# Kernel optimization log

Measured on AMD Instinct MI355X. Metric: run time of the kernel, lower is better.

The kernel has to match this reference:

```python
import jax, jax.numpy as jnp
import numpy as np

N = 8192      # number of tree nodes
IN = 1024     # in_dim
M = 1024      # effective mem_dim = 2 * mem_dim_init
K = 8         # max children (complete 8-ary tree)


def _linear_init(key, out_dim, in_dim):
    k1, k2 = jax.random.split(key)
    s = 1.0 / np.sqrt(in_dim)
    w = jax.random.uniform(k1, (out_dim, in_dim), minval=-s, maxval=s, dtype=jnp.float32)
    b = jax.random.uniform(k2, (out_dim,), minval=-s, maxval=s, dtype=jnp.float32)
    return w, b


def setup_inputs() -> dict:
    key = jax.random.key(0)
    ks = jax.random.split(key, 5)
    w_ioux, b_ioux = _linear_init(ks[0], 3 * M, IN)
    w_iouh, b_iouh = _linear_init(ks[1], 3 * M, M)
    w_fx, b_fx = _linear_init(ks[2], M, IN)
    w_fh, b_fh = _linear_init(ks[3], M, M)
    inputs = jax.random.normal(ks[4], (N, IN), dtype=jnp.float32)
    # Complete K-ary tree: children of node p are p*K+1 .. p*K+K (clipped).
    # Pad with index N, which addresses an always-zero dummy row.
    ch = np.full((N, K), N, dtype=np.int32)
    for j in range(K):
        idx = np.arange(N) * K + 1 + j
        valid = idx < N
        ch[valid, j] = idx[valid]
    return dict(inputs=inputs, children=jnp.asarray(ch),
                w_ioux=w_ioux, b_ioux=b_ioux, w_iouh=w_iouh, b_iouh=b_iouh,
                w_fx=w_fx, b_fx=b_fx, w_fh=w_fh, b_fh=b_fh)


def reference(inputs, children, w_ioux, b_ioux, w_iouh, b_iouh, w_fx, b_fx, w_fh, b_fh):
    # Precompute the input-side projections for all nodes at once.
    iou_x = inputs @ w_ioux.T + b_ioux   # [N, 3M]
    fx_x = inputs @ w_fx.T + b_fx        # [N, M]
    h0 = jnp.zeros((N + 1, M), inputs.dtype)  # row N is the zero pad slot
    c0 = jnp.zeros((N + 1, M), inputs.dtype)

    def step(carry, t):
        h_buf, c_buf = carry
        ch = children[t]           # [K] child indices (pad = N -> zero rows)
        ch_h = h_buf[ch]           # [K, M] real child h's
        ch_c = c_buf[ch]           # [K, M] real child c's
        # Faithful to original: for internal nodes child_c/child_h are SWAPPED,
        # so the 'child_h_sum' and f-gate inputs use the real c's, while the
        # forgotten memory (fc) multiplies the real h's. Leaves: all zeros.
        csum = ch_c.sum(0)                                   # [M]
        iou = iou_x[t] + csum @ w_iouh.T + b_iouh            # [3M]
        i_g, o_g, u_g = jnp.split(iou, 3)
        i_g = jax.nn.sigmoid(i_g)
        o_g = jax.nn.sigmoid(o_g)
        u_g = jnp.tanh(u_g)
        f = jax.nn.sigmoid(ch_c @ w_fh.T + b_fh + fx_x[t])   # [K, M]
        c = i_g * u_g + (f * ch_h).sum(0)                    # [M]
        h = o_g * jnp.tanh(c)
        return (h_buf.at[t].set(h), c_buf.at[t].set(c)), None

    # Children always have larger indices than their parent, so processing
    # t = N-1 .. 0 matches the original reverse-BFS (leaves-first) order.
    order = jnp.arange(N - 1, -1, -1)
    (h_buf, c_buf), _ = jax.lax.scan(step, (h0, c0), order)
    root_h = h_buf[0][None, :]   # [1, M]
    root_c = c_buf[0][None, :]   # [1, M]
    return root_h, root_c
```

## Files before the change

kernel.cpp:

```cpp
#include <hip/hip_runtime.h>

typedef __bf16 bf16x8 __attribute__((ext_vector_type(8)));
typedef __attribute__((ext_vector_type(4))) float f4;

#define AS1 __attribute__((address_space(1)))
#define AS3 __attribute__((address_space(3)))

__device__ __forceinline__ unsigned short f2bf(float f) {
    union { float f; unsigned int u; } x; x.f = f;
    return (unsigned short)((x.u + 0x7fffu + ((x.u >> 16) & 1u)) >> 16);
}
__device__ __forceinline__ float bf2f(unsigned short u) {
    union { unsigned int u; float f; } x; x.u = (unsigned int)u << 16;
    return x.f;
}
__device__ __forceinline__ float fsigm(float x) {
    return __builtin_amdgcn_rcpf(1.f + __expf(-x));
}
__device__ __forceinline__ float ftanh(float x) {
    return 1.f - 2.f * __builtin_amdgcn_rcpf(1.f + __expf(2.f * x));
}
__device__ __forceinline__ void gload_lds16(const unsigned short* g, unsigned short* l) {
    __builtin_amdgcn_global_load_lds((const AS1 unsigned int*)g, (AS3 unsigned int*)l, 16, 0, 0);
}

__global__ void prep_all_k(const float* __restrict__ inputs, const float* __restrict__ w_ioux,
                           const float* __restrict__ w_fx, const float* __restrict__ w_iouh,
                           const float* __restrict__ w_fh,
                           const float* __restrict__ b_ioux, const float* __restrict__ b_iouh,
                           const float* __restrict__ b_fx, const float* __restrict__ b_fh,
                           unsigned short* __restrict__ Xbf, unsigned short* __restrict__ Wiouxbf,
                           unsigned short* __restrict__ Wfxbf, unsigned short* __restrict__ Whbf,
                           unsigned short* __restrict__ Wfhbf,
                           float* __restrict__ bias_iou, float* __restrict__ bias_f,
                           unsigned short* __restrict__ c_bf, unsigned short* __restrict__ h_bf) {
    int b = blockIdx.x;
    if (b < 16384) {
        int idx = b * 256 + threadIdx.x;
        const float* src; unsigned short* dst; int rel;
        if (idx < 2097152)      { src = inputs; dst = Xbf;     rel = idx; }
        else if (idx < 2883584) { src = w_ioux; dst = Wiouxbf; rel = idx - 2097152; }
        else if (idx < 3145728) { src = w_fx;   dst = Wfxbf;   rel = idx - 2883584; }
        else if (idx < 3932160) { src = w_iouh; dst = Whbf;    rel = idx - 3145728; }
        else                    { src = w_fh;   dst = Wfhbf;   rel = idx - 3932160; }
        float4 v = reinterpret_cast<const float4*>(src)[rel];
        ushort4 o; o.x = f2bf(v.x); o.y = f2bf(v.y); o.z = f2bf(v.z); o.w = f2bf(v.w);
        reinterpret_cast<ushort4*>(dst)[rel] = o;
    } else if (b < 16400) {
        int idx = (b - 16384) * 256 + threadIdx.x;
        if (idx < 3072) bias_iou[idx] = b_ioux[idx] + b_iouh[idx];
        else { int j = idx - 3072; bias_f[j] = b_fx[j] + b_fh[j]; }
    } else {
        int j = (b - 16400) * 256 + threadIdx.x;
        size_t o = (size_t)8192 * 1024 + j;
        c_bf[o] = 0; h_bf[o] = 0;
    }
}

__device__ __forceinline__ void gemm_core_db(const unsigned short* __restrict__ A,
                                             const unsigned short* __restrict__ B,
                                             int M, int tile_m, int tile_n, int kb, int nsteps,
                                             unsigned short* lsA, unsigned short* lsB,
                                             f4 acc[4][4]) {
    const int K = 1024;
    const int tid = threadIdx.x;
    const int l = tid & 63, wid = tid >> 6;
    const int wm = wid >> 1, wn = wid & 1;
    const int fr = l & 15, q = l >> 4;

#pragma unroll
    for (int i = 0; i < 4; ++i)
#pragma unroll
        for (int j = 0; j < 4; ++j) acc[i][j] = (f4){0.f, 0.f, 0.f, 0.f};

    const unsigned short* ga[4]; const unsigned short* gb[4];
    unsigned short *la[4], *lb[4];
#pragma unroll
    for (int i = 0; i < 4; ++i) {
        int chunk = i * 256 + tid;
        int row = chunk >> 3, slot = chunk & 7;
        int scol = (slot ^ (row & 7)) * 8;
        ga[i] = A + (size_t)min(tile_m + row, M - 1) * K + kb * 64 + scol;
        gb[i] = B + (size_t)(tile_n + row) * K + kb * 64 + scol;
        la[i] = lsA + chunk * 8;
        lb[i] = lsB + chunk * 8;
    }
#pragma unroll
    for (int i = 0; i < 4; ++i) gload_lds16(ga[i], la[i]);
#pragma unroll
    for (int i = 0; i < 4; ++i) gload_lds16(gb[i], lb[i]);

    int roffA[4], roffB[4];
#pragma unroll
    for (int f = 0; f < 4; ++f) {
        roffA[f] = (wm * 64 + f * 16 + fr) * 64;
        roffB[f] = (wn * 64 + f * 16 + fr) * 64;
    }
    const int sw = fr & 7;
    int cur = 0;
    for (int t = 0; t < nsteps; ++t) {
        if (t < nsteps - 1) {
            int k0 = (t + 1) * 64;
            int nb = (cur ^ 1) * 8192;
#pragma unroll
            for (int i = 0; i < 4; ++i) gload_lds16(ga[i] + k0, la[i] + nb);
#pragma unroll
            for (int i = 0; i < 4; ++i) gload_lds16(gb[i] + k0, lb[i] + nb);
            asm volatile("s_waitcnt vmcnt(8)" ::: "memory");
        } else {
            asm volatile("s_waitcnt vmcnt(0)" ::: "memory");
        }
        __builtin_amdgcn_s_barrier();
        const unsigned short* bA = lsA + cur * 8192;
        const unsigned short* bB = lsB + cur * 8192;
        bf16x8 af[4][2], bq[4][2];
#pragma unroll
        for (int f = 0; f < 4; ++f)
#pragma unroll
            for (int s = 0; s < 2; ++s) {
                int sl = ((s * 4 + q) ^ sw) * 8;
                af[f][s] = *reinterpret_cast<const bf16x8*>(&bA[roffA[f] + sl]);
                bq[f][s] = *reinterpret_cast<const bf16x8*>(&bB[roffB[f] + sl]);
            }
#pragma unroll
        for (int s = 0; s < 2; ++s)
#pragma unroll
            for (int i = 0; i < 4; ++i)
#pragma unroll
                for (int j = 0; j < 4; ++j)
                    acc[i][j] = __builtin_amdgcn_mfma_f32_16x16x32_bf16(af[i][s], bq[j][s], acc[i][j], 0, 0, 0);
        __builtin_amdgcn_s_barrier();
        cur ^= 1;
    }
}

__global__ __launch_bounds__(256)
void gemm_big_k(const unsigned short* __restrict__ Xbf, const unsigned short* __restrict__ Wioux,
                const unsigned short* __restrict__ Wfx,
                const float* __restrict__ bias_iou, const float* __restrict__ bias_f,
                unsigned short* __restrict__ P_iou, unsigned short* __restrict__ P_f) {
    __shared__ unsigned short lsA[16384];
    __shared__ unsigned short lsB[16384];
    int b = blockIdx.x;
    const unsigned short* Bp; unsigned short* Cp; const float* biasp;
    int ldc, tm, tn, M;
    if (b < 1536) {
        tm = (b & 63) * 128; tn = (b >> 6) * 128;
        Bp = Wioux; Cp = P_iou; biasp = bias_iou; ldc = 3072; M = 8192;
    } else {
        int bb = b - 1536;
        tm = (bb & 7) * 128; tn = (bb >> 3) * 128;
        Bp = Wfx; Cp = P_f; biasp = bias_f; ldc = 1024; M = 1024;
    }
    f4 acc[4][4];
    gemm_core_db(Xbf, Bp, M, tm, tn, 0, 16, lsA, lsB, acc);

    const int l = threadIdx.x & 63, wid = threadIdx.x >> 6;
    const int wm = wid >> 1, wn = wid & 1;
    const int fr = l & 15, q = l >> 4;
#pragma unroll
    for (int i = 0; i < 4; ++i)
#pragma unroll
        for (int j = 0; j < 4; ++j) {
            int col = tn + wn * 64 + fr + j * 16;
            float bv = biasp[col];
#pragma unroll
            for (int r = 0; r < 4; ++r) {
                int row = tm + wm * 64 + q * 4 + i * 16 + r;
                Cp[(size_t)row * ldc + col] = f2bf(acc[i][j][r] + bv);
            }
        }
}

__global__ void leaf_act_k(const unsigned short* __restrict__ P_iou,
                           unsigned short* __restrict__ h_bf, unsigned short* __restrict__ c_bf) {
    int idx = blockIdx.x * blockDim.x + threadIdx.x;
    int t = 1024 + (idx >> 8);
    int j = (idx & 255) * 4;
    const unsigned short* p = P_iou + (size_t)t * 3072 + j;
    ushort4 pi = *reinterpret_cast<const ushort4*>(p);
    ushort4 po = *reinterpret_cast<const ushort4*>(p + 1024);
    ushort4 pu = *reinterpret_cast<const ushort4*>(p + 2048);
    ushort4 cb, hb;
    float c0, c1, c2, c3;
    c0 = fsigm(bf2f(pi.x)) * ftanh(bf2f(pu.x)); hb.x = f2bf(fsigm(bf2f(po.x)) * ftanh(c0)); cb.x = f2bf(c0);
    c1 = fsigm(bf2f(pi.y)) * ftanh(bf2f(pu.y)); hb.y = f2bf(fsigm(bf2f(po.y)) * ftanh(c1)); cb.y = f2bf(c1);
    c2 = fsigm(bf2f(pi.z)) * ftanh(bf2f(pu.z)); hb.z = f2bf(fsigm(bf2f(po.z)) * ftanh(c2)); cb.z = f2bf(c2);
    c3 = fsigm(bf2f(pi.w)) * ftanh(bf2f(pu.w)); hb.w = f2bf(fsigm(bf2f(po.w)) * ftanh(c3)); cb.w = f2bf(c3);
    size_t o = (size_t)t * 1024 + j;
    *reinterpret_cast<ushort4*>(c_bf + o) = cb;
    *reinterpret_cast<ushort4*>(h_bf + o) = hb;
}

__device__ __forceinline__ void csum_dev(const unsigned short* __restrict__ c_bf,
                                         unsigned short* __restrict__ csum_bf, int lo, int w) {
    int tt = w >> 8, j = (w & 255) * 4;
    int t = lo + tt;
    size_t base = (size_t)(t * 8 + 1) * 1024 + j;
    float s0 = 0.f, s1 = 0.f, s2 = 0.f, s3 = 0.f;
#pragma unroll
    for (int k = 0; k < 8; ++k) {
        ushort4 v = *reinterpret_cast<const ushort4*>(c_bf + base + (size_t)k * 1024);
        s0 += bf2f(v.x); s1 += bf2f(v.y); s2 += bf2f(v.z); s3 += bf2f(v.w);
    }
    ushort4 o; o.x = f2bf(s0); o.y = f2bf(s1); o.z = f2bf(s2); o.w = f2bf(s3);
    *reinterpret_cast<ushort4*>(csum_bf + (size_t)t * 1024 + j) = o;
}

__global__ void csum_k(const unsigned short* __restrict__ c_bf, unsigned short* __restrict__ csum_bf,
                       int lo, int n) {
    int w = blockIdx.x * blockDim.x + threadIdx.x;
    if (w < n * 256) csum_dev(c_bf, csum_bf, lo, w);
}

__global__ void node_update_k(const unsigned short* __restrict__ P_iou,
                              const unsigned short* __restrict__ P_f,
                              const float* __restrict__ out_iouh, const float* __restrict__ out_f,
                              unsigned short* __restrict__ h_bf, unsigned short* __restrict__ c_bf,
                              float* __restrict__ out, int lo, int n) {
    int w = blockIdx.x * blockDim.x + threadIdx.x;
    if (w >= n * 256) return;
    int tt = w >> 8, j = (w & 255) * 4;
    int t = lo + tt;
    const unsigned short* p = P_iou + (size_t)t * 3072 + j;
    ushort4 pi4 = *reinterpret_cast<const ushort4*>(p);
    ushort4 po4 = *reinterpret_cast<const ushort4*>(p + 1024);
    ushort4 pu4 = *reinterpret_cast<const ushort4*>(p + 2048);
    const float* oi = out_iouh + (size_t)tt * 3072 + j;
    f4 oii = *reinterpret_cast<const f4*>(oi);
    f4 oio = *reinterpret_cast<const f4*>(oi + 1024);
    f4 oiu = *reinterpret_cast<const f4*>(oi + 2048);
    ushort4 pf4 = *reinterpret_cast<const ushort4*>(P_f + (size_t)t * 1024 + j);
    float pf[4] = {bf2f(pf4.x), bf2f(pf4.y), bf2f(pf4.z), bf2f(pf4.w)};
    float a[4], og[4];
    a[0] = fsigm(bf2f(pi4.x) + oii[0]) * ftanh(bf2f(pu4.x) + oiu[0]);
    a[1] = fsigm(bf2f(pi4.y) + oii[1]) * ftanh(bf2f(pu4.y) + oiu[1]);
    a[2] = fsigm(bf2f(pi4.z) + oii[2]) * ftanh(bf2f(pu4.z) + oiu[2]);
    a[3] = fsigm(bf2f(pi4.w) + oii[3]) * ftanh(bf2f(pu4.w) + oiu[3]);
    og[0] = fsigm(bf2f(po4.x) + oio[0]);
    og[1] = fsigm(bf2f(po4.y) + oio[1]);
    og[2] = fsigm(bf2f(po4.z) + oio[2]);
    og[3] = fsigm(bf2f(po4.w) + oio[3]);
#pragma unroll
    for (int k = 0; k < 8; ++k) {
        f4 fo = *reinterpret_cast<const f4*>(out_f + (size_t)(tt * 8 + k) * 1024 + j);
        ushort4 hc = *reinterpret_cast<const ushort4*>(h_bf + (size_t)(t * 8 + 1 + k) * 1024 + j);
        a[0] += fsigm(pf[0] + fo[0]) * bf2f(hc.x);
        a[1] += fsigm(pf[1] + fo[1]) * bf2f(hc.y);
        a[2] += fsigm(pf[2] + fo[2]) * bf2f(hc.z);
        a[3] += fsigm(pf[3] + fo[3]) * bf2f(hc.w);
    }
    float h0 = og[0] * ftanh(a[0]);
    float h1 = og[1] * ftanh(a[1]);
    float h2 = og[2] * ftanh(a[2]);
    float h3 = og[3] * ftanh(a[3]);
    size_t o = (size_t)t * 1024 + j;
    ushort4 cb; cb.x = f2bf(a[0]); cb.y = f2bf(a[1]); cb.z = f2bf(a[2]); cb.w = f2bf(a[3]);
    ushort4 hb; hb.x = f2bf(h0); hb.y = f2bf(h1); hb.z = f2bf(h2); hb.w = f2bf(h3);
    *reinterpret_cast<ushort4*>(c_bf + o) = cb;
    *reinterpret_cast<ushort4*>(h_bf + o) = hb;
    if (t == 0) {
        f4 hv = {h0, h1, h2, h3};
        f4 cv = {a[0], a[1], a[2], a[3]};
        *reinterpret_cast<f4*>(out + j) = hv;
        *reinterpret_cast<f4*>(out + 1024 + j) = cv;
    }
}

struct GDesc {
    const unsigned short* A;
    const unsigned short* B;
    float* C;
    int M;
    int ldc;
    int tiles_n;
    int tiles_total;
};

__global__ __launch_bounds__(256)
void gemm_dual_k(GDesc d0, GDesc d1) {
    __shared__ unsigned short lsA[16384];
    __shared__ unsigned short lsB[16384];
    int b = blockIdx.x;
    GDesc d; int bb;
    if (b < d0.tiles_total) { d = d0; bb = b; }
    else { d = d1; bb = b - d0.tiles_total; }
    const int tile_m = (bb / d.tiles_n) * 128;
    const int tile_n = (bb % d.tiles_n) * 128;
    f4 acc[4][4];
    gemm_core_db(d.A, d.B, d.M, tile_m, tile_n, 0, 16, lsA, lsB, acc);

    const int l = threadIdx.x & 63, wid = threadIdx.x >> 6;
    const int wm = wid >> 1, wn = wid & 1;
    const int fr = l & 15, q = l >> 4;
#pragma unroll
    for (int i = 0; i < 4; ++i)
#pragma unroll
        for (int j = 0; j < 4; ++j) {
            int col = tile_n + wn * 64 + fr + j * 16;
#pragma unroll
            for (int r = 0; r < 4; ++r) {
                int row = tile_m + wm * 64 + q * 4 + i * 16 + r;
                if (row < d.M) d.C[(size_t)row * d.ldc + col] = acc[i][j][r];
            }
        }
}

__global__ __launch_bounds__(256)
void gemm_tail_k(const unsigned short* __restrict__ csum_lvl,
                 const unsigned short* __restrict__ cchild,
                 const unsigned short* __restrict__ Whbf, const unsigned short* __restrict__ Wfhbf,
                 float* __restrict__ part_iouh, float* __restrict__ part_f, int n) {
    __shared__ unsigned short lsA[16384];
    __shared__ unsigned short lsB[16384];
    int b = blockIdx.x;
    const unsigned short* A; const unsigned short* Bw; float* C;
    int M, ldc, tm, tn, split;
    if (b < 96) {
        split = b & 3; int tile = b >> 2;
        A = csum_lvl; Bw = Whbf; M = n; ldc = 3072; tm = 0; tn = tile * 128;
        C = part_iouh + (size_t)split * 64 * 3072;
    } else {
        int bb = b - 96;
        split = bb & 3; int tile = bb >> 2;
        A = cchild; Bw = Wfhbf; M = 8 * n; ldc = 1024;
        tm = (tile >> 3) * 128; tn = (tile & 7) * 128;
        C = part_f + (size_t)split * 512 * 1024;
    }
    f4 acc[4][4];
    gemm_core_db(A, Bw, M, tm, tn, split * 4, 4, lsA, lsB, acc);

    const int l = threadIdx.x & 63, wid = threadIdx.x >> 6;
    const int wm = wid >> 1, wn = wid & 1;
    const int fr = l & 15, q = l >> 4;
#pragma unroll
    for (int i = 0; i < 4; ++i)
#pragma unroll
        for (int j = 0; j < 4; ++j) {
            int col = tn + wn * 64 + fr + j * 16;
#pragma unroll
            for (int r = 0; r < 4; ++r) {
                int row = tm + wm * 64 + q * 4 + i * 16 + r;
                if (row < M) C[(size_t)row * ldc + col] = acc[i][j][r];
            }
        }
}

__global__ void node_update_tail_k(const unsigned short* __restrict__ P_iou,
                                   const unsigned short* __restrict__ P_f,
                                   const float* __restrict__ part_iouh,
                                   const float* __restrict__ part_f,
                                   unsigned short* __restrict__ h_bf, unsigned short* __restrict__ c_bf,
                                   float* __restrict__ out, int lo, int n) {
    int w = blockIdx.x * blockDim.x + threadIdx.x;
    if (w >= n * 256) return;
    int tt = w >> 8, j = (w & 255) * 4;
    int t = lo + tt;
    f4 oii = {0.f, 0.f, 0.f, 0.f}, oio = oii, oiu = oii;
#pragma unroll
    for (int s = 0; s < 4; ++s) {
        const float* base = part_iouh + (size_t)s * 64 * 3072 + (size_t)tt * 3072 + j;
        oii += *reinterpret_cast<const f4*>(base);
        oio += *reinterpret_cast<const f4*>(base + 1024);
        oiu += *reinterpret_cast<const f4*>(base + 2048);
    }
    const unsigned short* p = P_iou + (size_t)t * 3072 + j;
    ushort4 pi4 = *reinterpret_cast<const ushort4*>(p);
    ushort4 po4 = *reinterpret_cast<const ushort4*>(p + 1024);
    ushort4 pu4 = *reinterpret_cast<const ushort4*>(p + 2048);
    ushort4 pf4 = *reinterpret_cast<const ushort4*>(P_f + (size_t)t * 1024 + j);
    float pf[4] = {bf2f(pf4.x), bf2f(pf4.y), bf2f(pf4.z), bf2f(pf4.w)};
    float a[4], og[4];
    a[0] = fsigm(bf2f(pi4.x) + oii[0]) * ftanh(bf2f(pu4.x) + oiu[0]);
    a[1] = fsigm(bf2f(pi4.y) + oii[1]) * ftanh(bf2f(pu4.y) + oiu[1]);
    a[2] = fsigm(bf2f(pi4.z) + oii[2]) * ftanh(bf2f(pu4.z) + oiu[2]);
    a[3] = fsigm(bf2f(pi4.w) + oii[3]) * ftanh(bf2f(pu4.w) + oiu[3]);
    og[0] = fsigm(bf2f(po4.x) + oio[0]);
    og[1] = fsigm(bf2f(po4.y) + oio[1]);
    og[2] = fsigm(bf2f(po4.z) + oio[2]);
    og[3] = fsigm(bf2f(po4.w) + oio[3]);
#pragma unroll
    for (int k = 0; k < 8; ++k) {
        f4 fo = {0.f, 0.f, 0.f, 0.f};
#pragma unroll
        for (int s = 0; s < 4; ++s)
            fo += *reinterpret_cast<const f4*>(part_f + (size_t)s * 512 * 1024 +
                                               (size_t)(tt * 8 + k) * 1024 + j);
        ushort4 hc = *reinterpret_cast<const ushort4*>(h_bf + (size_t)(t * 8 + 1 + k) * 1024 + j);
        a[0] += fsigm(pf[0] + fo[0]) * bf2f(hc.x);
        a[1] += fsigm(pf[1] + fo[1]) * bf2f(hc.y);
        a[2] += fsigm(pf[2] + fo[2]) * bf2f(hc.z);
        a[3] += fsigm(pf[3] + fo[3]) * bf2f(hc.w);
    }
    float h0 = og[0] * ftanh(a[0]);
    float h1 = og[1] * ftanh(a[1]);
    float h2 = og[2] * ftanh(a[2]);
    float h3 = og[3] * ftanh(a[3]);
    size_t o = (size_t)t * 1024 + j;
    ushort4 cb; cb.x = f2bf(a[0]); cb.y = f2bf(a[1]); cb.z = f2bf(a[2]); cb.w = f2bf(a[3]);
    ushort4 hb; hb.x = f2bf(h0); hb.y = f2bf(h1); hb.z = f2bf(h2); hb.w = f2bf(h3);
    *reinterpret_cast<ushort4*>(c_bf + o) = cb;
    *reinterpret_cast<ushort4*>(h_bf + o) = hb;
    if (t == 0) {
        f4 hv = {h0, h1, h2, h3};
        f4 cv = {a[0], a[1], a[2], a[3]};
        *reinterpret_cast<f4*>(out + j) = hv;
        *reinterpret_cast<f4*>(out + 1024 + j) = cv;
    }
}

extern "C" void kernel_launch(void* const* d_in, const int* in_sizes, int n_in,
                              void* d_out, int out_size, void* d_ws, size_t ws_size,
                              hipStream_t stream) {
    const float* inputs = (const float*)d_in[0];
    const float* w_ioux = (const float*)d_in[2];
    const float* b_ioux = (const float*)d_in[3];
    const float* w_iouh = (const float*)d_in[4];
    const float* b_iouh = (const float*)d_in[5];
    const float* w_fx   = (const float*)d_in[6];
    const float* b_fx   = (const float*)d_in[7];
    const float* w_fh   = (const float*)d_in[8];
    const float* b_fh   = (const float*)d_in[9];
    float* out = (float*)d_out;

    char* ws = (char*)d_ws;
    size_t off = 0;
    auto alloc = [&](size_t bytes) -> void* {
        void* p = ws + off;
        off += (bytes + 255) & ~(size_t)255;
        return p;
    };
    unsigned short* Xbf     = (unsigned short*)alloc((size_t)8192 * 1024 * 2);
    unsigned short* Wiouxbf = (unsigned short*)alloc((size_t)3072 * 1024 * 2);
    unsigned short* Wfxbf   = (unsigned short*)alloc((size_t)1024 * 1024 * 2);
    unsigned short* Whbf    = (unsigned short*)alloc((size_t)3072 * 1024 * 2);
    unsigned short* Wfhbf   = (unsigned short*)alloc((size_t)1024 * 1024 * 2);
    float* bias_iou         = (float*)alloc((size_t)3072 * 4);
    float* bias_f           = (float*)alloc((size_t)1024 * 4);
    unsigned short* P_iou   = (unsigned short*)alloc((size_t)8192 * 3072 * 2);
    unsigned short* P_f     = (unsigned short*)alloc((size_t)1024 * 1024 * 2);
    unsigned short* c_bf    = (unsigned short*)alloc((size_t)8193 * 1024 * 2);
    unsigned short* h_bf    = (unsigned short*)alloc((size_t)8193 * 1024 * 2);
    unsigned short* csum_bf = (unsigned short*)alloc((size_t)1024 * 1024 * 2);
    float* out_iouh         = (float*)alloc((size_t)512 * 3072 * 4);
    float* out_f            = (float*)alloc((size_t)4096 * 1024 * 4);
    float* part_iouh        = (float*)alloc((size_t)4 * 64 * 3072 * 4);
    float* part_f           = (float*)alloc((size_t)4 * 512 * 1024 * 4);

    prep_all_k<<<dim3(16404), dim3(256), 0, stream>>>(
        inputs, w_ioux, w_fx, w_iouh, w_fh, b_ioux, b_iouh, b_fx, b_fh,
        Xbf, Wiouxbf, Wfxbf, Whbf, Wfhbf, bias_iou, bias_f, c_bf, h_bf);

    gemm_big_k<<<dim3(1600), dim3(256), 0, stream>>>(Xbf, Wiouxbf, Wfxbf,
                                                     bias_iou, bias_f, P_iou, P_f);
    leaf_act_k<<<dim3(7168), dim3(256), 0, stream>>>(P_iou, h_bf, c_bf);
    csum_k<<<dim3(896), dim3(256), 0, stream>>>(c_bf, csum_bf, 128, 896);

    {
        const int lo = 585, n = 439;
        GDesc d0, d1;
        d0.A = csum_bf + (size_t)lo * 1024; d0.B = Whbf; d0.C = out_iouh;
        d0.M = n; d0.ldc = 3072; d0.tiles_n = 24;
        d0.tiles_total = ((n + 127) / 128) * 24;
        d1.A = c_bf + (size_t)(lo * 8 + 1) * 1024; d1.B = Wfhbf; d1.C = out_f;
        d1.M = 8 * n; d1.ldc = 1024; d1.tiles_n = 8;
        d1.tiles_total = ((8 * n + 127) / 128) * 8;
        gemm_dual_k<<<dim3(d0.tiles_total + d1.tiles_total), dim3(256), 0, stream>>>(d0, d1);
        node_update_k<<<dim3(n), dim3(256), 0, stream>>>(
            P_iou, P_f, out_iouh, out_f, h_bf, c_bf, out, lo, n);
    }
    {
        const int lo = 73, n = 512;
        csum_k<<<dim3(55), dim3(256), 0, stream>>>(c_bf, csum_bf, 73, 55);
        GDesc d0, d1;
        d0.A = csum_bf + (size_t)lo * 1024; d0.B = Whbf; d0.C = out_iouh;
        d0.M = n; d0.ldc = 3072; d0.tiles_n = 24;
        d0.tiles_total = ((n + 127) / 128) * 24;
        d1.A = c_bf + (size_t)(lo * 8 + 1) * 1024; d1.B = Wfhbf; d1.C = out_f;
        d1.M = 8 * n; d1.ldc = 1024; d1.tiles_n = 8;
        d1.tiles_total = ((8 * n + 127) / 128) * 8;
        gemm_dual_k<<<dim3(d0.tiles_total + d1.tiles_total), dim3(256), 0, stream>>>(d0, d1);
        node_update_k<<<dim3(n), dim3(256), 0, stream>>>(
            P_iou, P_f, out_iouh, out_f, h_bf, c_bf, out, lo, n);
    }
    const int T_LO[3] = {9, 1, 0};
    const int T_N[3]  = {64, 8, 1};
    for (int lv = 0; lv < 3; ++lv) {
        int lo = T_LO[lv], n = T_N[lv];
        csum_k<<<dim3(n), dim3(256), 0, stream>>>(c_bf, csum_bf, lo, n);
        int fm_tiles = (8 * n + 127) / 128;
        int nblk = 96 + fm_tiles * 8 * 4;
        gemm_tail_k<<<dim3(nblk), dim3(256), 0, stream>>>(
            csum_bf + (size_t)lo * 1024, c_bf + (size_t)(lo * 8 + 1) * 1024,
            Whbf, Wfhbf, part_iouh, part_f, n);
        node_update_tail_k<<<dim3(n), dim3(256), 0, stream>>>(
            P_iou, P_f, part_iouh, part_f, h_bf, c_bf, out, lo, n);
    }
    (void)in_sizes; (void)n_in; (void)out_size; (void)ws_size;
}
```

Baseline: 219.5 us.

## Rewrite input-projection GEMM with 256x256 tiles, 8 waves and interleaved prefetch

Replaces the 128x128, 4-wave input projection GEMM with a 256x256-tile, 512-thread kernel. It uses a 128KB LDS double buffer, XOR-swizzled direct-to-LDS loads, and a fine-grained interleave of half-tile prefetches between MFMA groups, raising MFMA priority during compute. Block indices are remapped so consecutive workgroups spread across XCD-style groups for cache locality. The aim is more data reuse per tile and hiding global-load latency behind compute. The cost is heavy LDS use that limits occupancy, many barriers, and fewer blocks (400), which may leave CUs underused.

```diff
diff --git a/kernel.cpp b/kernel.cpp
--- a/kernel.cpp
+++ b/kernel.cpp
@@ -22,6 +22,11 @@
 }
 __device__ __forceinline__ void gload_lds16(const unsigned short* g, unsigned short* l) {
     __builtin_amdgcn_global_load_lds((const AS1 unsigned int*)g, (AS3 unsigned int*)l, 16, 0, 0);
+}
+__device__ __forceinline__ void bar() {
+    asm volatile("" ::: "memory");
+    __builtin_amdgcn_s_barrier();
+    asm volatile("" ::: "memory");
 }
 
 __global__ void prep_all_k(const float* __restrict__ inputs, const float* __restrict__ w_ioux,
@@ -57,6 +62,151 @@
     }
 }
 
+__device__ __forceinline__ void stage_half(const unsigned short* __restrict__ G, int trow0, int kt,
+                                           unsigned short* lds_region, int tid) {
+#pragma unroll
+    for (int ii = 0; ii < 2; ++ii) {
+        int c = ii * 512 + tid;
+        int r = c >> 3, sl = c & 7;
+        gload_lds16(G + (size_t)(trow0 + r) * 1024 + kt * 64 + ((sl ^ (r & 7)) * 8),
+                    lds_region + c * 8);
+    }
+}
+__device__ __forceinline__ bf16x8 rdfrag(const unsigned short* region, int rowih, int kslot) {
+    return *reinterpret_cast<const bf16x8*>(&region[rowih * 64 + ((kslot ^ (rowih & 7)) * 8)]);
+}
+
+#define RD_A(AF, REG, FB)                                                        \
+    _Pragma("unroll") for (int f_ = 0; f_ < 4; ++f_)                             \
+    _Pragma("unroll") for (int s_ = 0; s_ < 2; ++s_)                             \
+        (AF)[f_][s_] = rdfrag((REG), ((FB) + f_) * 16 + fr, s_ * 4 + q);
+#define RD_B(BQ, REG, GB)                                                        \
+    _Pragma("unroll") for (int g_ = 0; g_ < 2; ++g_)                             \
+    _Pragma("unroll") for (int s_ = 0; s_ < 2; ++s_)                             \
+        (BQ)[g_][s_] = rdfrag((REG), bcol0 + ((GB) + g_) * 16 + fr, s_ * 4 + q);
+#define MF16(FB, GB, AF, BQ)                                                     \
+    __builtin_amdgcn_s_setprio(1);                                               \
+    _Pragma("unroll") for (int s_ = 0; s_ < 2; ++s_)                             \
+    _Pragma("unroll") for (int f_ = 0; f_ < 4; ++f_)                             \
+    _Pragma("unroll") for (int g_ = 0; g_ < 2; ++g_)                             \
+        acc[(FB) + f_][(GB) + g_] = __builtin_amdgcn_mfma_f32_16x16x32_bf16(     \
+            (AF)[f_][s_], (BQ)[g_][s_], acc[(FB) + f_][(GB) + g_], 0, 0, 0);     \
+    __builtin_amdgcn_s_setprio(0);
+
+__global__ __launch_bounds__(512, 2)
+void gemm_big_k(const unsigned short* __restrict__ Xbf, const unsigned short* __restrict__ Wioux,
+                const unsigned short* __restrict__ Wfx,
+                const float* __restrict__ bias_iou, const float* __restrict__ bias_f,
+                unsigned short* __restrict__ P_iou, unsigned short* __restrict__ P_f) {
+    __shared__ unsigned short ls[65536];
+    int b = blockIdx.x;
+    b = (b & 7) * 50 + (b >> 3);
+    const unsigned short* Am; const unsigned short* Bm; unsigned short* Cp; const float* biasp;
+    int tm, tn, ldc;
+    if (b < 384) {
+        tm = (b & 31) * 256; tn = (b >> 5) * 256;
+        Am = Xbf; Bm = Wioux; Cp = P_iou; biasp = bias_iou; ldc = 3072;
+    } else {
+        int bb = b - 384;
+        tm = (bb & 3) * 256; tn = (bb >> 2) * 256;
+        Am = Xbf; Bm = Wfx; Cp = P_f; biasp = bias_f; ldc = 1024;
+    }
+    const int tid = threadIdx.x;
+    const int l = tid & 63, w = tid >> 6;
+    const int wm = w >> 2, wn = w & 3;
+    const int fr = l & 15, q = l >> 4;
+    const int bcol0 = (wn & 1) * 64;
+
+    unsigned short* S0 = ls;
+    unsigned short* S1 = ls + 32768;
+    const unsigned short* Ar0 = S0 + wm * 8192;
+    const unsigned short* Br0 = S0 + (2 + (wn >> 1)) * 8192;
+    const unsigned short* Ar1 = S1 + wm * 8192;
+    const unsigned short* Br1 = S1 + (2 + (wn >> 1)) * 8192;
+
+    f4 acc[8][4];
+#pragma unroll
+    for (int i = 0; i < 8; ++i)
+#pragma unroll
+        for (int j = 0; j < 4; ++j) acc[i][j] = (f4){0.f, 0.f, 0.f, 0.f};
+
+    stage_half(Am, tm,       0, S0 + 0 * 8192, tid);
+    stage_half(Am, tm + 128, 0, S0 + 1 * 8192, tid);
+    stage_half(Bm, tn,       0, S0 + 2 * 8192, tid);
+    stage_half(Bm, tn + 128, 0, S0 + 3 * 8192, tid);
+    stage_half(Bm, tn,       1, S1 + 2 * 8192, tid);
+    stage_half(Bm, tn + 128, 1, S1 + 3 * 8192, tid);
+    asm volatile("s_waitcnt vmcnt(4)" ::: "memory");
+    bar();
+
+    for (int i = 0; i < 8; ++i) {
+        bf16x8 afA[4][2], afB[4][2], bq01[2][2], bq23[2][2];
+        RD_A(afA, Ar0, 0)
+        RD_B(bq01, Br0, 0)
+        stage_half(Am, tm,       2 * i + 1, S1 + 0 * 8192, tid);
+        bar();
+        MF16(0, 0, afA, bq01)
+        bar();
+        RD_B(bq23, Br0, 2)
+        stage_half(Am, tm + 128, 2 * i + 1, S1 + 1 * 8192, tid);
+        bar();
+        MF16(0, 2, afA, bq23)
+        bar();
+        RD_A(afB, Ar0, 4)
+        if (i < 7) stage_half(Bm, tn,       2 * i + 2, S0 + 2 * 8192, tid);
+        bar();
+        MF16(4, 2, afB, bq23)
+        bar();
+        if (i < 7) {
+            stage_half(Bm, tn + 128, 2 * i + 2, S0 + 3 * 8192, tid);
+            asm volatile("s_waitcnt vmcnt(4)" ::: "memory");
+        } else {
+            asm volatile("s_waitcnt vmcnt(0)" ::: "memory");
+        }
+        bar();
+        MF16(4, 0, afB, bq01)
+        bar();
+        RD_A(afA, Ar1, 0)
+        RD_B(bq01, Br1, 0)
+        if (i < 7) stage_half(Am, tm,       2 * i + 2, S0 + 0 * 8192, tid);
+        bar();
+        MF16(0, 0, afA, bq01)
+        bar();
+        RD_B(bq23, Br1, 2)
+        if (i < 7) stage_half(Am, tm + 128, 2 * i + 2, S0 + 1 * 8192, tid);
+        bar();
+        MF16(0, 2, afA, bq23)
+        bar();
+        RD_A(afB, Ar1, 4)
+        if (i < 7) stage_half(Bm, tn,       2 * i + 3, S1 + 2 * 8192, tid);
+        bar();
+        MF16(4, 2, afB, bq23)
+        bar();
+        if (i < 7) {
+            stage_half(Bm, tn + 128, 2 * i + 3, S1 + 3 * 8192, tid);
+            asm volatile("s_waitcnt vmcnt(4)" ::: "memory");
+        } else {
+            asm volatile("s_waitcnt vmcnt(0)" ::: "memory");
+        }
+        bar();
+        MF16(4, 0, afB, bq01)
+        bar();
+    }
+
+#pragma unroll
+    for (int f = 0; f < 8; ++f)
+#pragma unroll
+        for (int g = 0; g < 4; ++g) {
+            int col = tn + wn * 64 + g * 16 + fr;
+            float bv = biasp[col];
+#pragma unroll
+            for (int r = 0; r < 4; ++r) {
+                int row = tm + wm * 128 + f * 16 + q * 4 + r;
+                Cp[(size_t)row * ldc + col] = f2bf(acc[f][g][r] + bv);
+            }
+        }
+}
+
 __device__ __forceinline__ void gemm_core_db(const unsigned short* __restrict__ A,
                                              const unsigned short* __restrict__ B,
                                              int M, int tile_m, int tile_n, int kb, int nsteps,
@@ -132,44 +282,6 @@
         __builtin_amdgcn_s_barrier();
         cur ^= 1;
     }
-}
-
-__global__ __launch_bounds__(256)
-void gemm_big_k(const unsigned short* __restrict__ Xbf, const unsigned short* __restrict__ Wioux,
-                const unsigned short* __restrict__ Wfx,
-                const float* __restrict__ bias_iou, const float* __restrict__ bias_f,
-                unsigned short* __restrict__ P_iou, unsigned short* __restrict__ P_f) {
-    __shared__ unsigned short lsA[16384];
-    __shared__ unsigned short lsB[16384];
-    int b = blockIdx.x;
-    const unsigned short* Bp; unsigned short* Cp; const float* biasp;
-    int ldc, tm, tn, M;
-    if (b < 1536) {
-        tm = (b & 63) * 128; tn = (b >> 6) * 128;
-        Bp = Wioux; Cp = P_iou; biasp = bias_iou; ldc = 3072; M = 8192;
-    } else {
-        int bb = b - 1536;
-        tm = (bb & 7) * 128; tn = (bb >> 3) * 128;
-        Bp = Wfx; Cp = P_f; biasp = bias_f; ldc = 1024; M = 1024;
-    }
-    f4 acc[4][4];
-    gemm_core_db(Xbf, Bp, M, tm, tn, 0, 16, lsA, lsB, acc);
-
-    const int l = threadIdx.x & 63, wid = threadIdx.x >> 6;
-    const int wm = wid >> 1, wn = wid & 1;
-    const int fr = l & 15, q = l >> 4;
-#pragma unroll
-    for (int i = 0; i < 4; ++i)
-#pragma unroll
-        for (int j = 0; j < 4; ++j) {
-            int col = tn + wn * 64 + fr + j * 16;
-            float bv = biasp[col];
-#pragma unroll
-            for (int r = 0; r < 4; ++r) {
-                int row = tm + wm * 64 + q * 4 + i * 16 + r;
-                Cp[(size_t)row * ldc + col] = f2bf(acc[i][j][r] + bv);
-            }
-        }
 }
 
 __global__ void leaf_act_k(const unsigned short* __restrict__ P_iou,
@@ -451,8 +563,8 @@
         inputs, w_ioux, w_fx, w_iouh, w_fh, b_ioux, b_iouh, b_fx, b_fh,
         Xbf, Wiouxbf, Wfxbf, Whbf, Wfhbf, bias_iou, bias_f, c_bf, h_bf);
 
-    gemm_big_k<<<dim3(1600), dim3(256), 0, stream>>>(Xbf, Wiouxbf, Wfxbf,
-                                                     bias_iou, bias_f, P_iou, P_f);
+    gemm_big_k<<<dim3(400), dim3(512), 0, stream>>>(Xbf, Wiouxbf, Wfxbf,
+                                                    bias_iou, bias_f, P_iou, P_f);
     leaf_act_k<<<dim3(7168), dim3(256), 0, stream>>>(P_iou, h_bf, c_bf);
     csum_k<<<dim3(896), dim3(256), 0, stream>>>(c_bf, csum_bf, 128, 896);
 
```

Result: faster. 206.6 us (-5.9%).
